# Kernel tuning notes

Measured on AMD Instinct MI355X. Metric: run time of the kernel, lower is better.

Reference implementation:

```python
import jax, jax.numpy as jnp
from jax import lax
import numpy as np

B, R, NOBJ, SIZE = 16, 64, 32, 64  # batch, rels/image, objs/image, map size


def setup_inputs() -> dict:
    key = jax.random.key(0)
    ks = jax.random.split(key, 8)
    # boxes as (x1, y1, x2, y2) in an arbitrary image coordinate frame
    xy1 = jax.random.uniform(ks[0], (B, NOBJ, 2), dtype=jnp.float32) * 80.0
    wh = jax.random.uniform(ks[1], (B, NOBJ, 2), dtype=jnp.float32) * 40.0 + 2.0
    bboxes = jnp.concatenate([xy1, xy1 + wh], axis=-1)  # [B, NOBJ, 4]
    num_obj = jnp.full((B,), NOBJ, dtype=jnp.int32)
    num_relation = jnp.full((B,), R, dtype=jnp.int32)  # constant -> static tot_num_rels
    object_pairs = jax.random.randint(ks[2], (B, R, 2), 0, NOBJ)
    conv1_w = jax.random.normal(ks[3], (64, 2, 5, 5), dtype=jnp.float32) * 0.1
    conv1_b = jnp.zeros((64,), dtype=jnp.float32)
    conv2_w = jax.random.normal(ks[4], (32, 64, 5, 5), dtype=jnp.float32) * 0.05
    conv2_b = jnp.zeros((32,), dtype=jnp.float32)
    fc_w = jax.random.normal(ks[5], (512, 32), dtype=jnp.float32) * 0.1
    fc_b = jnp.zeros((512,), dtype=jnp.float32)
    return dict(bboxes=bboxes, num_obj=num_obj, num_relation=num_relation,
                object_pairs=object_pairs, conv1_w=conv1_w, conv1_b=conv1_b,
                conv2_w=conv2_w, conv2_b=conv2_b, fc_w=fc_w, fc_b=fc_b)


def _sp_maps(bboxes, object_pairs):
    # Vectorized replacement of the per-relation python loop + get_sp:
    # both boxes of a pair are rescaled into the 64x64 frame of their union
    # box and rasterized as binary masks (iCAN-style 2-channel spatial config).
    Bc, Rc, _ = object_pairs.shape
    pairs = object_pairs.reshape(-1, 2)                      # [T, 2]
    b_idx = jnp.repeat(jnp.arange(Bc), Rc)                   # [T]
    b0 = bboxes[b_idx, pairs[:, 0]]                          # [T, 4]
    b1 = bboxes[b_idx, pairs[:, 1]]                          # [T, 4]
    ux1 = jnp.minimum(b0[:, 0], b1[:, 0])
    uy1 = jnp.minimum(b0[:, 1], b1[:, 1])
    ux2 = jnp.maximum(b0[:, 2], b1[:, 2])
    uy2 = jnp.maximum(b0[:, 3], b1[:, 3])
    uw = jnp.maximum(ux2 - ux1, 1e-6)
    uh = jnp.maximum(uy2 - uy1, 1e-6)

    def scale(b):  # union-normalized box in [0, SIZE] grid coords
        return jnp.stack([(b[:, 0] - ux1) / uw * SIZE,
                          (b[:, 1] - uy1) / uh * SIZE,
                          (b[:, 2] - ux1) / uw * SIZE,
                          (b[:, 3] - uy1) / uh * SIZE], axis=-1)

    coords = jnp.arange(SIZE, dtype=jnp.float32) + 0.5
    gx = coords[None, None, :]   # [1, 1, SIZE]
    gy = coords[None, :, None]   # [1, SIZE, 1]

    def rasterize(sb):  # sb: [T, 4] -> [T, SIZE, SIZE]
        x1 = sb[:, 0, None, None]; y1 = sb[:, 1, None, None]
        x2 = sb[:, 2, None, None]; y2 = sb[:, 3, None, None]
        return ((gx >= x1) & (gx <= x2) & (gy >= y1) & (gy <= y2)).astype(jnp.float32)

    return jnp.stack([rasterize(scale(b0)), rasterize(scale(b1))], axis=1)  # [T,2,64,64]


def _conv(x, w, b):
    y = lax.conv_general_dilated(x, w, window_strides=(1, 1), padding='VALID',
                                 dimension_numbers=('NCHW', 'OIHW', 'NCHW'))
    return y + b[None, :, None, None]


def _maxpool2(x):
    return lax.reduce_window(x, -jnp.inf, lax.max, (1, 1, 2, 2), (1, 1, 2, 2), 'VALID')


def reference(bboxes, num_obj, num_relation, object_pairs,
              conv1_w, conv1_b, conv2_w, conv2_b, fc_w, fc_b):
    sp = _sp_maps(bboxes, object_pairs)        # [T, 2, 64, 64]
    x = _maxpool2(_conv(sp, conv1_w, conv1_b)) # [T, 64, 30, 30]
    x = _maxpool2(_conv(x, conv2_w, conv2_b))  # [T, 32, 13, 13]
    x = jnp.mean(x, axis=(2, 3))               # AvgPool((13,13)) -> [T, 32]
    return jax.nn.relu(x @ fc_w.T + fc_b)      # [T, 512]
```

## Files before the change

### kernel.cpp

```cpp
#include <hip/hip_runtime.h>
#include <stdint.h>

typedef unsigned long long u64;
typedef short v8s __attribute__((ext_vector_type(8)));
typedef float v4f __attribute__((ext_vector_type(4)));

__device__ __forceinline__ unsigned short f2bf_rne(float f) {
  union { float f; unsigned u; } c; c.f = f;
  unsigned u = c.u;
  u += 0x7fffu + ((u >> 16) & 1u);
  return (unsigned short)(u >> 16);
}

__device__ __forceinline__ void bacc(uint4 z, uint4 a, float* S) {
  const unsigned* zp = &z.x;
  const unsigned* ap = &a.x;
  #pragma unroll
  for (int k = 0; k < 4; k++) {
    unsigned zu = zp[k], au = ap[k];
    S[2 * k]     += __uint_as_float(zu << 16)         - __uint_as_float(au << 16);
    S[2 * k + 1] += __uint_as_float(zu & 0xffff0000u) - __uint_as_float(au & 0xffff0000u);
  }
}


__global__ __launch_bounds__(512, 8) void conv1_kernel(
    const float* __restrict__ bboxes,
    const int*   __restrict__ pairs,
    const float* __restrict__ w1,
    const float* __restrict__ b1,
    const float* __restrict__ w2,
    unsigned short* __restrict__ XsG,
    unsigned short* __restrict__ Wr)
{
  const int t = threadIdx.x;
  if (blockIdx.x >= 1024) {
    int bb2 = blockIdx.x - 1024;
    #pragma unroll
    for (int r = 0; r < 4; r++) {
      int idx = bb2 * 2048 + r * 512 + t;
      int c = idx / 1600, rem = idx - c * 1600;
      int h = rem / 800, r2 = rem - h * 800;
      int tap = r2 >> 5, chh = r2 & 31;
      Wr[h * 25600 + c * 800 + r2] =
          f2bf_rne(w2[(c * 64 + h * 32 + chh) * 25 + tap]);
    }
    return;
  }
  extern __shared__ char smem[];
  unsigned short* Gs = (unsigned short*)smem;
  float* R = (float*)(smem + 24576);

  const int n = blockIdx.x;
  const int lane = t & 63;

  for (int rid = t; rid < 640; rid += 512) {
    int ch = rid / 320, rr = rid - ch * 320;
    int i = rr >> 6, cout = rr & 63;
    const float* wp = w1 + (cout * 2 + ch) * 25 + i * 5;
    float* Rp = R + (ch * 5 + i) * 384 + cout;
    float s = 0.f;
    #pragma unroll
    for (int j = 0; j < 5; j++) { Rp[j * 64] = s; s += wp[j]; }
    Rp[5 * 64] = s;
  }
  __syncthreads();
  for (int e = t; e < 12288; e += 512) {
    int ch = e / 6144, r = e - ch * 6144;
    int cls = r / 384, r2 = r - cls * 384;
    float v = 0.f;
    if (cls > 0) {
      int ia = 0, ib = 0;
      #pragma unroll
      for (int bb2 = 0; bb2 < 5; bb2++) {
        int base = (bb2 * (bb2 + 1)) / 2 + 1;
        if (cls >= base) { ib = bb2; ia = cls - base; }
      }
      const float* Rp = R + ch * 1920 + r2;
      for (int i = ia; i <= ib; i++) v += Rp[i * 384];
    }
    Gs[e] = f2bf_rne(v);
  }

  const int bb = n >> 6, rr_ = n & 63;
  const int p0 = pairs[(bb * 64 + rr_) * 2 + 0];
  const int p1 = pairs[(bb * 64 + rr_) * 2 + 1];
  const float* A  = bboxes + (bb * 32 + p0) * 4;
  const float* Bq = bboxes + (bb * 32 + p1) * 4;
  const float ax1 = A[0],  ay1 = A[1],  ax2 = A[2],  ay2 = A[3];
  const float cx1 = Bq[0], cy1 = Bq[1], cx2 = Bq[2], cy2 = Bq[3];
  const float ux1 = fminf(ax1, cx1), uy1 = fminf(ay1, cy1);
  const float ux2 = fmaxf(ax2, cx2), uy2 = fmaxf(ay2, cy2);
  const float uw = fmaxf(ux2 - ux1, 1e-6f), uh = fmaxf(uy2 - uy1, 1e-6f);
  const float g = (float)lane + 0.5f;
  u64 ixs[2], iys[2];
  {
    float X1 = (ax1 - ux1) / uw * 64.f, X2 = (ax2 - ux1) / uw * 64.f;
    float Y1 = (ay1 - uy1) / uh * 64.f, Y2 = (ay2 - uy1) / uh * 64.f;
    ixs[0] = __ballot(g >= X1 && g <= X2);
    iys[0] = __ballot(g >= Y1 && g <= Y2);
  }
  {
    float X1 = (cx1 - ux1) / uw * 64.f, X2 = (cx2 - ux1) / uw * 64.f;
    float Y1 = (cy1 - uy1) / uh * 64.f, Y2 = (cy2 - uy1) / uh * 64.f;
    ixs[1] = __ballot(g >= X1 && g <= X2);
    iys[1] = __ballot(g >= Y1 && g <= Y2);
  }
  __syncthreads();

  const int cg = t & 7, cgo = cg * 16, pr = t >> 3;
  const int hW = cg >> 2;
  float b1v[8];
  #pragma unroll
  for (int i = 0; i < 8; i++) b1v[i] = b1[cg * 8 + i];
  char* const Xbase = (char*)XsG + (u64)n * 115200 + hW * 57600;
  for (int pass = 0; pass < 15; pass++) {
    int pix = pr + (pass << 6);
    if (pix < 900) {
      int qy = pix / 30, qx = pix - qy * 30;
      int cb[2][2], ja_[2][2], jb_[2][2];
      #pragma unroll
      for (int ch = 0; ch < 2; ch++) {
        #pragma unroll
        for (int dy = 0; dy < 2; dy++) {
          unsigned m = (unsigned)(iys[ch] >> (2 * qy + dy)) & 31u;
          int ia = __ffs((int)m) - 1; if (ia < 0) ia = 0;
          int ib = 31 - __clz((int)(m | 1u));
          int cls = m ? (((ib * (ib + 1)) >> 1) + ia + 1) : 0;
          cb[ch][dy] = (ch * 16 + cls) * 768 + cgo;
        }
        #pragma unroll
        for (int dx = 0; dx < 2; dx++) {
          unsigned mx = (unsigned)(ixs[ch] >> (2 * qx + dx)) & 31u;
          int ja = __ffs((int)mx) - 1; if (ja < 0) ja = 0;
          int jbp = mx ? (32 - __clz((int)mx)) : 0;
          ja_[ch][dx] = ja * 128; jb_[ch][dx] = jbp * 128;
        }
      }
      float V[8];
      #pragma unroll
      for (int dy = 0; dy < 2; dy++) {
        #pragma unroll
        for (int dx = 0; dx < 2; dx++) {
          float S[8] = {0, 0, 0, 0, 0, 0, 0, 0};
          #pragma unroll
          for (int ch = 0; ch < 2; ch++) {
            uint4 z = *(const uint4*)(smem + cb[ch][dy] + jb_[ch][dx]);
            uint4 a = *(const uint4*)(smem + cb[ch][dy] + ja_[ch][dx]);
            bacc(z, a, S);
          }
          #pragma unroll
          for (int k = 0; k < 8; k++)
            V[k] = (dy == 0 && dx == 0) ? S[k] : fmaxf(V[k], S[k]);
        }
      }
      uint4 pk;
      unsigned* pkp = &pk.x;
      #pragma unroll
      for (int k = 0; k < 4; k++) {
        unsigned lo = (unsigned)f2bf_rne(V[2 * k]     + b1v[2 * k]);
        unsigned hi = (unsigned)f2bf_rne(V[2 * k + 1] + b1v[2 * k + 1]);
        pkp[k] = lo | (hi << 16);
      }
      int slot = ((cg & 3) + pix) & 3;
      *(uint4*)(Xbase + pix * 64 + slot * 16) = pk;
    }
  }
}

__global__ __launch_bounds__(512, 4) void conv2_kernel(
    const unsigned short* __restrict__ XsG,
    const unsigned short* __restrict__ Wr,
    const float* __restrict__ b2,
    const float* __restrict__ fcw,
    const float* __restrict__ fcb,
    float* __restrict__ out)
{
  extern __shared__ char smem[];
  float* partial = (float*)(smem + 57600);
  float* fs      = (float*)(smem + 58432);
  float* Cout    = (float*)smem;

  const int n = blockIdx.x, t = threadIdx.x;
  const int lane = t & 63, wv = t >> 6;
  const int q = lane >> 4, ln = lane & 15;

  v4f acc[6][2];
  int pclamp[6], psB[6];
  int cnt = 0;
  #pragma unroll
  for (int it = 0; it < 6; it++) {
    int nt = wv + it * 8;
    if (nt < 43) {
      int p = nt * 16 + ln; if (p > 675) p = 675;
      pclamp[it] = p;
      int y = p / 26, x = p - y * 26;
      psB[it] = y * 30 + x;
      cnt = it + 1;
    } else { pclamp[it] = 0; psB[it] = 0; }
    acc[it][0] = (v4f)0.f; acc[it][1] = (v4f)0.f;
  }

  const char* Xg = (const char*)XsG + (u64)n * 115200;
  for (int h = 0; h < 2; h++) {
    if (h) __syncthreads();
    {
      const char* src = Xg + h * 57600;
      #pragma unroll
      for (int k = 0; k < 7; k++) {
        int ci = k * 512 + t;
        __builtin_amdgcn_global_load_lds(
            (const __attribute__((address_space(1))) unsigned int*)(src + ci * 16),
            (__attribute__((address_space(3))) unsigned int*)(smem + ci * 16),
            16, 0, 0);
      }
      if (t < 16) {
        int ci = 3584 + t;
        __builtin_amdgcn_global_load_lds(
            (const __attribute__((address_space(1))) unsigned int*)(src + ci * 16),
            (__attribute__((address_space(3))) unsigned int*)(smem + ci * 16),
            16, 0, 0);
      }
    }
    __syncthreads();

    const unsigned short* pA0 = Wr + h * 25600 + ln * 800 + q * 8;
    const unsigned short* pA1 = pA0 + 16 * 800;
    for (int i = 0; i < 5; i++) {
      #pragma unroll
      for (int j = 0; j < 5; j++) {
        const int tap = i * 5 + j;
        v8s a0 = *(const v8s*)(pA0 + tap * 32);
        v8s a1 = *(const v8s*)(pA1 + tap * 32);
        #pragma unroll
        for (int it = 0; it < 6; it++) {
          if (it < cnt) {
            int ps = psB[it] + i * 30 + j;
            int addr = (ps << 6) + (((q + ps) & 3) << 4);
            v8s b = *(const v8s*)(smem + addr);
            acc[it][0] = __builtin_amdgcn_mfma_f32_16x16x32_bf16(a0, b, acc[it][0], 0, 0, 0);
            acc[it][1] = __builtin_amdgcn_mfma_f32_16x16x32_bf16(a1, b, acc[it][1], 0, 0, 0);
          }
        }
      }
    }
  }

  #pragma unroll
  for (int mt = 0; mt < 2; mt++) {
    __syncthreads();
    #pragma unroll
    for (int it = 0; it < 6; it++) {
      if (it < cnt) {
        #pragma unroll
        for (int r = 0; r < 4; r++)
          Cout[(q * 4 + r) * 677 + pclamp[it]] = acc[it][mt][r];
      }
    }
    __syncthreads();
    if (t < 208) {
      int c = t & 15, py = t >> 4;
      const float* r0 = Cout + c * 677 + (2 * py) * 26;
      const float* r1 = r0 + 26;
      float s = 0.f;
      #pragma unroll
      for (int px = 0; px < 13; px++) {
        float m0 = fmaxf(r0[2 * px], r0[2 * px + 1]);
        float m1 = fmaxf(r1[2 * px], r1[2 * px + 1]);
        s += fmaxf(m0, m1);
      }
      partial[t] = s;
    }
    __syncthreads();
    if (t < 16) {
      float s = 0.f;
      #pragma unroll
      for (int k = 0; k < 13; k++) s += partial[k * 16 + t];
      fs[mt * 16 + t] = s * (1.f / 169.f) + b2[mt * 16 + t];
    }
  }
  __syncthreads();

  {
    const float* wrow = fcw + t * 32;
    float d = 0.f;
    #pragma unroll
    for (int k = 0; k < 32; k++) d += wrow[k] * fs[k];
    out[(u64)n * 512 + t] = fmaxf(d + fcb[t], 0.f);
  }
}


__global__ __launch_bounds__(256) void prepack(
    const float* __restrict__ w1, const float* __restrict__ w2,
    unsigned short* __restrict__ Wr, unsigned short* __restrict__ Gt) {
  int idx = blockIdx.x * 256 + threadIdx.x;
  if (idx < 51200) {
    int c = idx / 1600, rem = idx - c * 1600;
    int ch = rem & 63, tap = rem >> 6;
    Wr[idx] = f2bf_rne(w2[(c * 64 + ch) * 25 + tap]);
  } else if (idx < 51200 + 12288) {
    int e = idx - 51200;
    int ch = e / 6144, r = e - ch * 6144;
    int cls = r / 384, r2 = r - cls * 384;
    int j = r2 / 64, cout = r2 - j * 64;
    float v = 0.f;
    if (cls > 0) {
      int ia = 0, ib = 0;
      for (int bb = 0; bb < 5; bb++) {
        int base = (bb * (bb + 1)) / 2 + 1;
        if (cls >= base && cls <= base + bb) { ib = bb; ia = cls - base; }
      }
      for (int i = ia; i <= ib; i++)
        for (int jj = 0; jj < j; jj++)
          v += w1[(cout * 2 + ch) * 25 + i * 5 + jj];
    }
    Gt[e] = f2bf_rne(v);
  }
}

__global__ __launch_bounds__(512, 2) void fused_kernel(
    const float* __restrict__ bboxes, const int* __restrict__ pairs,
    const unsigned short* __restrict__ Gt, const float* __restrict__ b1,
    const unsigned short* __restrict__ Wr, const float* __restrict__ b2,
    const float* __restrict__ fcw, const float* __restrict__ fcb,
    float* __restrict__ out)
{
  extern __shared__ char smem[];
  float* partial = (float*)(smem + 146976);
  float* fs      = (float*)(smem + 147808);
  float* Cout    = (float*)smem;

  const int n = blockIdx.x, t = threadIdx.x;
  const int lane = t & 63, wv = t >> 6;
  const int q = lane >> 4, ln = lane & 15;

  {
    const uint4* src = (const uint4*)Gt;
    uint4* dst = (uint4*)(smem + 122400);
    #pragma unroll
    for (int i = 0; i < 3; i++) dst[t + i * 512] = src[t + i * 512];
  }
  const int bb = n >> 6, rr_ = n & 63;
  const int p0 = pairs[(bb * 64 + rr_) * 2 + 0];
  const int p1 = pairs[(bb * 64 + rr_) * 2 + 1];
  const float* A  = bboxes + (bb * 32 + p0) * 4;
  const float* Bq = bboxes + (bb * 32 + p1) * 4;
  const float ax1 = A[0],  ay1 = A[1],  ax2 = A[2],  ay2 = A[3];
  const float cx1 = Bq[0], cy1 = Bq[1], cx2 = Bq[2], cy2 = Bq[3];
  const float ux1 = fminf(ax1, cx1), uy1 = fminf(ay1, cy1);
  const float ux2 = fmaxf(ax2, cx2), uy2 = fmaxf(ay2, cy2);
  const float uw = fmaxf(ux2 - ux1, 1e-6f), uh = fmaxf(uy2 - uy1, 1e-6f);
  const float g = (float)lane + 0.5f;
  u64 ixs[2], iys[2];
  {
    float X1 = (ax1 - ux1) / uw * 64.f, X2 = (ax2 - ux1) / uw * 64.f;
    float Y1 = (ay1 - uy1) / uh * 64.f, Y2 = (ay2 - uy1) / uh * 64.f;
    ixs[0] = __ballot(g >= X1 && g <= X2);
    iys[0] = __ballot(g >= Y1 && g <= Y2);
  }
  {
    float X1 = (cx1 - ux1) / uw * 64.f, X2 = (cx2 - ux1) / uw * 64.f;
    float Y1 = (cy1 - uy1) / uh * 64.f, Y2 = (cy2 - uy1) / uh * 64.f;
    ixs[1] = __ballot(g >= X1 && g <= X2);
    iys[1] = __ballot(g >= Y1 && g <= Y2);
  }
  __syncthreads();

  {
    const int cg = t & 7, cgo = cg * 16, pr = t >> 3;
    float b1v[8];
    #pragma unroll
    for (int i = 0; i < 8; i++) b1v[i] = b1[cg * 8 + i];
    for (int pass = 0; pass < 15; pass++) {
      int pix = pr + (pass << 6);
      if (pix < 900) {
        int qy = pix / 30, qx = pix - qy * 30;
        int cb[2][2], ja_[2][2], jb_[2][2];
        #pragma unroll
        for (int ch = 0; ch < 2; ch++) {
          #pragma unroll
          for (int dy = 0; dy < 2; dy++) {
            unsigned m = (unsigned)(iys[ch] >> (2 * qy + dy)) & 31u;
            int ia = __ffs((int)m) - 1; if (ia < 0) ia = 0;
            int ib = 31 - __clz((int)(m | 1u));
            int cls = m ? (((ib * (ib + 1)) >> 1) + ia + 1) : 0;
            cb[ch][dy] = 122400 + (ch * 16 + cls) * 768 + cgo;
          }
          #pragma unroll
          for (int dx = 0; dx < 2; dx++) {
            unsigned mx = (unsigned)(ixs[ch] >> (2 * qx + dx)) & 31u;
            int ja = __ffs((int)mx) - 1; if (ja < 0) ja = 0;
            int jbp = mx ? (32 - __clz((int)mx)) : 0;
            ja_[ch][dx] = ja * 128; jb_[ch][dx] = jbp * 128;
          }
        }
        float V[8];
        #pragma unroll
        for (int dy = 0; dy < 2; dy++) {
          #pragma unroll
          for (int dx = 0; dx < 2; dx++) {
            float S[8] = {0, 0, 0, 0, 0, 0, 0, 0};
            #pragma unroll
            for (int ch = 0; ch < 2; ch++) {
              uint4 z = *(const uint4*)(smem + cb[ch][dy] + jb_[ch][dx]);
              uint4 a = *(const uint4*)(smem + cb[ch][dy] + ja_[ch][dx]);
              bacc(z, a, S);
            }
            #pragma unroll
            for (int k = 0; k < 8; k++)
              V[k] = (dy == 0 && dx == 0) ? S[k] : fmaxf(V[k], S[k]);
          }
        }
        unsigned dws[4];
        #pragma unroll
        for (int k = 0; k < 4; k++) {
          unsigned lo = (unsigned)f2bf_rne(V[2 * k]     + b1v[2 * k]);
          unsigned hi = (unsigned)f2bf_rne(V[2 * k + 1] + b1v[2 * k + 1]);
          dws[k] = lo | (hi << 16);
        }
        uint2 s0; s0.x = dws[0]; s0.y = dws[1];
        uint2 s1; s1.x = dws[2]; s1.y = dws[3];
        *(uint2*)(smem + pix * 136 + cgo) = s0;
        *(uint2*)(smem + pix * 136 + cgo + 8) = s1;
      }
    }
  }
  __syncthreads();

  v4f acc[6][2];
  int pclamp[6], baseB[6];
  int cnt = 0;
  #pragma unroll
  for (int it = 0; it < 6; it++) {
    int nt = wv + it * 8;
    if (nt < 43) {
      int p = nt * 16 + ln; if (p > 675) p = 675;
      pclamp[it] = p;
      int y = p / 26, x = p - y * 26;
      baseB[it] = (y * 30 + x) * 136 + q * 16;
      cnt = it + 1;
    } else { pclamp[it] = 0; baseB[it] = 0; }
    acc[it][0] = (v4f)0.f; acc[it][1] = (v4f)0.f;
  }
  const unsigned short* pA0 = Wr + ln * 1600 + q * 8;
  const unsigned short* pA1 = pA0 + 16 * 1600;
  for (int i5 = 0; i5 < 5; i5++) {
    const int ro = i5 * 4080;
    #pragma unroll
    for (int jt = 0; jt < 5; jt++) {
      #pragma unroll
      for (int hh = 0; hh < 2; hh++) {
        const int s = (i5 * 5 + jt) * 2 + hh;
        v8s a0 = *(const v8s*)(pA0 + s * 32);
        v8s a1 = *(const v8s*)(pA1 + s * 32);
        const int off = ro + jt * 136 + hh * 64;
        #pragma unroll
        for (int it = 0; it < 6; it++) {
          if (it < cnt) {
            uint2 lo = *(const uint2*)(smem + (baseB[it] + off));
            uint2 hi = *(const uint2*)(smem + (baseB[it] + off + 8));
            uint4 bv; bv.x = lo.x; bv.y = lo.y; bv.z = hi.x; bv.w = hi.y;
            v8s b = __builtin_bit_cast(v8s, bv);
            acc[it][0] = __builtin_amdgcn_mfma_f32_16x16x32_bf16(a0, b, acc[it][0], 0, 0, 0);
            acc[it][1] = __builtin_amdgcn_mfma_f32_16x16x32_bf16(a1, b, acc[it][1], 0, 0, 0);
          }
        }
      }
    }
  }
  #pragma unroll
  for (int mt = 0; mt < 2; mt++) {
    __syncthreads();
    #pragma unroll
    for (int it = 0; it < 6; it++) {
      if (it < cnt) {
        #pragma unroll
        for (int r = 0; r < 4; r++)
          Cout[(q * 4 + r) * 677 + pclamp[it]] = acc[it][mt][r];
      }
    }
    __syncthreads();
    if (t < 208) {
      int c = t & 15, py = t >> 4;
      const float* r0 = Cout + c * 677 + (2 * py) * 26;
      const float* r1 = r0 + 26;
      float s = 0.f;
      #pragma unroll
      for (int px = 0; px < 13; px++) {
        float m0 = fmaxf(r0[2 * px], r0[2 * px + 1]);
        float m1 = fmaxf(r1[2 * px], r1[2 * px + 1]);
        s += fmaxf(m0, m1);
      }
      partial[t] = s;
    }
    __syncthreads();
    if (t < 16) {
      float s = 0.f;
      #pragma unroll
      for (int k = 0; k < 13; k++) s += partial[k * 16 + t];
      fs[mt * 16 + t] = s * (1.f / 169.f) + b2[mt * 16 + t];
    }
  }
  __syncthreads();
  {
    const float* wrow = fcw + t * 32;
    float d = 0.f;
    #pragma unroll
    for (int k = 0; k < 32; k++) d += wrow[k] * fs[k];
    out[(u64)n * 512 + t] = fmaxf(d + fcb[t], 0.f);
  }
}

extern "C" void kernel_launch(void* const* d_in, const int* in_sizes, int n_in,
                              void* d_out, int out_size, void* d_ws, size_t ws_size,
                              hipStream_t stream) {
  const float* bboxes = (const float*)d_in[0];
  const int*   pairs  = (const int*)  d_in[3];
  const float* w1     = (const float*)d_in[4];
  const float* b1     = (const float*)d_in[5];
  const float* w2     = (const float*)d_in[6];
  const float* b2     = (const float*)d_in[7];
  const float* fcw    = (const float*)d_in[8];
  const float* fcb    = (const float*)d_in[9];
  float* out = (float*)d_out;

  const u64 xs_bytes = (u64)1024 * 115200;
  if (ws_size >= xs_bytes + 102400) {
    unsigned short* XsG = (unsigned short*)d_ws;
    unsigned short* Wr  = (unsigned short*)((char*)d_ws + xs_bytes);
    conv1_kernel<<<1049, 512, 39936, stream>>>(bboxes, pairs, w1, b1, w2, XsG, Wr);
    conv2_kernel<<<1024, 512, 58560, stream>>>(XsG, Wr, b2, fcw, fcb, out);
  } else {
    unsigned short* Wr = (unsigned short*)d_ws;
    unsigned short* Gt = (unsigned short*)((char*)d_ws + 102400);
    prepack<<<248, 256, 0, stream>>>(w1, w2, Wr, Gt);
    fused_kernel<<<1024, 512, 147936, stream>>>(bboxes, pairs, Gt, b1, Wr, b2,
                                                fcw, fcb, out);
  }
}
```

Baseline: 237.0 us.

## Switch conv2 to 32x32x16 MFMA with four 16-channel input chunks

Conv2 now uses the 32x32x16 bf16 MFMA covering all 32 output channels per instruction, instead of pairs of 16x16x32 MFMAs. The conv1 output and the weight prepacking are relaid into four 16-channel input-chunk slabs so each chunk fits in about 29KB of LDS. Halving LDS lets launch bounds rise to 6 blocks per CU, and each B-fragment load now feeds one larger MFMA. The trade-off is four staging rounds with extra syncs instead of two, and a pooling epilogue split into four groups.

Result: slower. 377.1 us (+59.1%).

```diff
diff --git a/kernel.cpp b/kernel.cpp
--- a/kernel.cpp
+++ b/kernel.cpp
@@ -4,6 +4,7 @@
 typedef unsigned long long u64;
 typedef short v8s __attribute__((ext_vector_type(8)));
 typedef float v4f __attribute__((ext_vector_type(4)));
+typedef float v16f __attribute__((ext_vector_type(16)));
 
 __device__ __forceinline__ unsigned short f2bf_rne(float f) {
   union { float f; unsigned u; } c; c.f = f;
@@ -39,11 +40,12 @@
     #pragma unroll
     for (int r = 0; r < 4; r++) {
       int idx = bb2 * 2048 + r * 512 + t;
-      int c = idx / 1600, rem = idx - c * 1600;
-      int h = rem / 800, r2 = rem - h * 800;
-      int tap = r2 >> 5, chh = r2 & 31;
-      Wr[h * 25600 + c * 800 + r2] =
-          f2bf_rne(w2[(c * 64 + h * 32 + chh) * 25 + tap]);
+      int j = idx & 7, v = idx >> 3;
+      int l = v & 63, tapq = v >> 6;
+      int tap = tapq % 25, qq = tapq / 25;
+      int m = l & 31, q2 = l >> 5;
+      int cin = qq * 16 + q2 * 8 + j;
+      Wr[idx] = f2bf_rne(w2[(m * 64 + cin) * 25 + tap]);
     }
     return;
   }
@@ -109,11 +111,11 @@
   __syncthreads();
 
   const int cg = t & 7, cgo = cg * 16, pr = t >> 3;
-  const int hW = cg >> 2;
+  const int qq = cg >> 1, sslot = cg & 1;
   float b1v[8];
   #pragma unroll
   for (int i = 0; i < 8; i++) b1v[i] = b1[cg * 8 + i];
-  char* const Xbase = (char*)XsG + (u64)n * 115200 + hW * 57600;
+  char* const Xbase = (char*)XsG + (u64)n * 115200 + qq * 28800;
   for (int pass = 0; pass < 15; pass++) {
     int pix = pr + (pass << 6);
     if (pix < 900) {
@@ -162,13 +164,13 @@
         unsigned hi = (unsigned)f2bf_rne(V[2 * k + 1] + b1v[2 * k + 1]);
         pkp[k] = lo | (hi << 16);
       }
-      int slot = ((cg & 3) + pix) & 3;
-      *(uint4*)(Xbase + pix * 64 + slot * 16) = pk;
-    }
-  }
-}
-
-__global__ __launch_bounds__(512, 4) void conv2_kernel(
+      int slot = (sslot + (pix >> 2)) & 1;
+      *(uint4*)(Xbase + pix * 32 + slot * 16) = pk;
+    }
+  }
+}
+
+__global__ __launch_bounds__(512, 6) void conv2_kernel(
     const unsigned short* __restrict__ XsG,
     const unsigned short* __restrict__ Wr,
     const float* __restrict__ b2,
@@ -177,45 +179,45 @@
     float* __restrict__ out)
 {
   extern __shared__ char smem[];
-  float* partial = (float*)(smem + 57600);
-  float* fs      = (float*)(smem + 58432);
-  float* Cout    = (float*)smem;
+  float* partial = (float*)(smem + 28800);
+  float* fs      = (float*)(smem + 29632);
+  float* Cout8   = (float*)smem;
 
   const int n = blockIdx.x, t = threadIdx.x;
   const int lane = t & 63, wv = t >> 6;
-  const int q = lane >> 4, ln = lane & 15;
-
-  v4f acc[6][2];
-  int pclamp[6], psB[6];
+  const int n31 = lane & 31, q2 = lane >> 5;
+
+  v16f acc[3];
+  int pclamp[3], psB[3];
   int cnt = 0;
   #pragma unroll
-  for (int it = 0; it < 6; it++) {
+  for (int it = 0; it < 3; it++) {
     int nt = wv + it * 8;
-    if (nt < 43) {
-      int p = nt * 16 + ln; if (p > 675) p = 675;
+    if (nt < 22) {
+      int p = nt * 32 + n31; if (p > 675) p = 675;
       pclamp[it] = p;
       int y = p / 26, x = p - y * 26;
       psB[it] = y * 30 + x;
       cnt = it + 1;
     } else { pclamp[it] = 0; psB[it] = 0; }
-    acc[it][0] = (v4f)0.f; acc[it][1] = (v4f)0.f;
+    acc[it] = (v16f)0.f;
   }
 
   const char* Xg = (const char*)XsG + (u64)n * 115200;
-  for (int h = 0; h < 2; h++) {
-    if (h) __syncthreads();
+  for (int qq = 0; qq < 4; qq++) {
+    if (qq) __syncthreads();
     {
-      const char* src = Xg + h * 57600;
-      #pragma unroll
-      for (int k = 0; k < 7; k++) {
+      const char* src = Xg + qq * 28800;
+      #pragma unroll
+      for (int k = 0; k < 3; k++) {
         int ci = k * 512 + t;
         __builtin_amdgcn_global_load_lds(
             (const __attribute__((address_space(1))) unsigned int*)(src + ci * 16),
             (__attribute__((address_space(3))) unsigned int*)(smem + ci * 16),
             16, 0, 0);
       }
-      if (t < 16) {
-        int ci = 3584 + t;
+      if (t < 264) {
+        int ci = 1536 + t;
         __builtin_amdgcn_global_load_lds(
             (const __attribute__((address_space(1))) unsigned int*)(src + ci * 16),
             (__attribute__((address_space(3))) unsigned int*)(smem + ci * 16),
@@ -224,22 +226,20 @@
     }
     __syncthreads();
 
-    const unsigned short* pA0 = Wr + h * 25600 + ln * 800 + q * 8;
-    const unsigned short* pA1 = pA0 + 16 * 800;
+    const unsigned short* pA = Wr + (u64)(qq * 25 * 64 + lane) * 8;
+    #pragma unroll
     for (int i = 0; i < 5; i++) {
       #pragma unroll
       for (int j = 0; j < 5; j++) {
         const int tap = i * 5 + j;
-        v8s a0 = *(const v8s*)(pA0 + tap * 32);
-        v8s a1 = *(const v8s*)(pA1 + tap * 32);
-        #pragma unroll
-        for (int it = 0; it < 6; it++) {
+        v8s a = *(const v8s*)(pA + tap * 512);
+        #pragma unroll
+        for (int it = 0; it < 3; it++) {
           if (it < cnt) {
-            int ps = psB[it] + i * 30 + j;
-            int addr = (ps << 6) + (((q + ps) & 3) << 4);
+            int p = psB[it] + i * 30 + j;
+            int addr = (p << 5) + (((q2 + (p >> 2)) & 1) << 4);
             v8s b = *(const v8s*)(smem + addr);
-            acc[it][0] = __builtin_amdgcn_mfma_f32_16x16x32_bf16(a0, b, acc[it][0], 0, 0, 0);
-            acc[it][1] = __builtin_amdgcn_mfma_f32_16x16x32_bf16(a1, b, acc[it][1], 0, 0, 0);
+            acc[it] = __builtin_amdgcn_mfma_f32_32x32x16_bf16(a, b, acc[it], 0, 0, 0);
           }
         }
       }
@@ -247,20 +247,20 @@
   }
 
   #pragma unroll
-  for (int mt = 0; mt < 2; mt++) {
-    __syncthreads();
-    #pragma unroll
-    for (int it = 0; it < 6; it++) {
+  for (int gp = 0; gp < 4; gp++) {
+    __syncthreads();
+    #pragma unroll
+    for (int it = 0; it < 3; it++) {
       if (it < cnt) {
         #pragma unroll
-        for (int r = 0; r < 4; r++)
-          Cout[(q * 4 + r) * 677 + pclamp[it]] = acc[it][mt][r];
-      }
-    }
-    __syncthreads();
-    if (t < 208) {
-      int c = t & 15, py = t >> 4;
-      const float* r0 = Cout + c * 677 + (2 * py) * 26;
+        for (int r4 = 0; r4 < 4; r4++)
+          Cout8[(r4 + 4 * q2) * 677 + pclamp[it]] = acc[it][gp * 4 + r4];
+      }
+    }
+    __syncthreads();
+    if (t < 104) {
+      int c = t & 7, py = t >> 3;
+      const float* r0 = Cout8 + c * 677 + (2 * py) * 26;
       const float* r1 = r0 + 26;
       float s = 0.f;
       #pragma unroll
@@ -272,11 +272,11 @@
       partial[t] = s;
     }
     __syncthreads();
-    if (t < 16) {
+    if (t < 8) {
       float s = 0.f;
       #pragma unroll
-      for (int k = 0; k < 13; k++) s += partial[k * 16 + t];
-      fs[mt * 16 + t] = s * (1.f / 169.f) + b2[mt * 16 + t];
+      for (int k = 0; k < 13; k++) s += partial[k * 8 + t];
+      fs[gp * 8 + t] = s * (1.f / 169.f) + b2[gp * 8 + t];
     }
   }
   __syncthreads();
@@ -530,7 +530,7 @@
     unsigned short* XsG = (unsigned short*)d_ws;
     unsigned short* Wr  = (unsigned short*)((char*)d_ws + xs_bytes);
     conv1_kernel<<<1049, 512, 39936, stream>>>(bboxes, pairs, w1, b1, w2, XsG, Wr);
-    conv2_kernel<<<1024, 512, 58560, stream>>>(XsG, Wr, b2, fcw, fcb, out);
+    conv2_kernel<<<1024, 512, 29760, stream>>>(XsG, Wr, b2, fcw, fcb, out);
   } else {
     unsigned short* Wr = (unsigned short*)d_ws;
     unsigned short* Gt = (unsigned short*)((char*)d_ws + 102400);
```

## Pad conv1 output rows to 72 bytes and stage stores through LDS

Applied to the files above, without the earlier changes.

The intermediate activation layout changes from a 64-byte rotated-slot pixel stride to a 72-byte padded stride per pixel. conv1 now writes each pass into a double-buffered LDS tile and then copies it out in contiguous 16-byte chunks, so global stores are coalesced instead of scattered per pixel. conv2 reads the padded layout with two 8-byte LDS loads per fragment to avoid bank conflicts without the XOR swizzle. The cost is more workspace and LDS, an extra barrier per pass in conv1, lower occupancy bounds, and split LDS loads in the MFMA inner loop.

Result: slower. 412.4 us (+74.0%).

```diff
diff --git a/kernel.cpp b/kernel.cpp
--- a/kernel.cpp
+++ b/kernel.cpp
@@ -24,7 +24,7 @@
 }
 
 
-__global__ __launch_bounds__(512, 8) void conv1_kernel(
+__global__ __launch_bounds__(512, 6) void conv1_kernel(
     const float* __restrict__ bboxes,
     const int*   __restrict__ pairs,
     const float* __restrict__ w1,
@@ -50,6 +50,7 @@
   extern __shared__ char smem[];
   unsigned short* Gs = (unsigned short*)smem;
   float* R = (float*)(smem + 24576);
+  char* const bufs = smem + 24576;
 
   const int n = blockIdx.x;
   const int lane = t & 63;
@@ -109,14 +110,17 @@
   __syncthreads();
 
   const int cg = t & 7, cgo = cg * 16, pr = t >> 3;
-  const int hW = cg >> 2;
+  const int h = cg >> 2, sub = cg & 3;
   float b1v[8];
   #pragma unroll
   for (int i = 0; i < 8; i++) b1v[i] = b1[cg * 8 + i];
-  char* const Xbase = (char*)XsG + (u64)n * 115200 + hW * 57600;
+  const u64 imgbase = (u64)n * 129600;
+
   for (int pass = 0; pass < 15; pass++) {
-    int pix = pr + (pass << 6);
-    if (pix < 900) {
+    const int cntpix = (pass == 14) ? 4 : 64;
+    char* buf = bufs + (pass & 1) * 9216;
+    if (pr < cntpix) {
+      int pix = pr + (pass << 6);
       int qy = pix / 30, qx = pix - qy * 30;
       int cb[2][2], ja_[2][2], jb_[2][2];
       #pragma unroll
@@ -162,8 +166,18 @@
         unsigned hi = (unsigned)f2bf_rne(V[2 * k + 1] + b1v[2 * k + 1]);
         pkp[k] = lo | (hi << 16);
       }
-      int slot = ((cg & 3) + pix) & 3;
-      *(uint4*)(Xbase + pix * 64 + slot * 16) = pk;
+      *(uint4*)(buf + h * 4608 + pr * 72 + sub * 16) = pk;
+    }
+    __syncthreads();
+    {
+      const int cph = (cntpix * 9) >> 1;
+      const int tot = cph * 2;
+      for (int idx = t; idx < tot; idx += 512) {
+        int hh = idx >= cph;
+        int off = (idx - hh * cph) * 16;
+        uint4 v = *(const uint4*)(buf + hh * 4608 + off);
+        *(uint4*)((char*)XsG + imgbase + (u64)hh * 64800 + pass * 4608 + off) = v;
+      }
     }
   }
 }
@@ -177,8 +191,8 @@
     float* __restrict__ out)
 {
   extern __shared__ char smem[];
-  float* partial = (float*)(smem + 57600);
-  float* fs      = (float*)(smem + 58432);
+  float* partial = (float*)(smem + 64800);
+  float* fs      = (float*)(smem + 65632);
   float* Cout    = (float*)smem;
 
   const int n = blockIdx.x, t = threadIdx.x;
@@ -186,7 +200,7 @@
   const int q = lane >> 4, ln = lane & 15;
 
   v4f acc[6][2];
-  int pclamp[6], psB[6];
+  int pclamp[6], baseB[6];
   int cnt = 0;
   #pragma unroll
   for (int it = 0; it < 6; it++) {
@@ -195,17 +209,17 @@
       int p = nt * 16 + ln; if (p > 675) p = 675;
       pclamp[it] = p;
       int y = p / 26, x = p - y * 26;
-      psB[it] = y * 30 + x;
+      baseB[it] = (y * 30 + x) * 72 + q * 16;
       cnt = it + 1;
-    } else { pclamp[it] = 0; psB[it] = 0; }
+    } else { pclamp[it] = 0; baseB[it] = 0; }
     acc[it][0] = (v4f)0.f; acc[it][1] = (v4f)0.f;
   }
 
-  const char* Xg = (const char*)XsG + (u64)n * 115200;
+  const char* Xg = (const char*)XsG + (u64)n * 129600;
   for (int h = 0; h < 2; h++) {
     if (h) __syncthreads();
     {
-      const char* src = Xg + h * 57600;
+      const char* src = Xg + h * 64800;
       #pragma unroll
       for (int k = 0; k < 7; k++) {
         int ci = k * 512 + t;
@@ -214,7 +228,7 @@
             (__attribute__((address_space(3))) unsigned int*)(smem + ci * 16),
             16, 0, 0);
       }
-      if (t < 16) {
+      if (t < 466) {
         int ci = 3584 + t;
         __builtin_amdgcn_global_load_lds(
             (const __attribute__((address_space(1))) unsigned int*)(src + ci * 16),
@@ -227,17 +241,20 @@
     const unsigned short* pA0 = Wr + h * 25600 + ln * 800 + q * 8;
     const unsigned short* pA1 = pA0 + 16 * 800;
     for (int i = 0; i < 5; i++) {
+      const int rowoff = i * 2160;
       #pragma unroll
       for (int j = 0; j < 5; j++) {
-        const int tap = i * 5 + j;
-        v8s a0 = *(const v8s*)(pA0 + tap * 32);
-        v8s a1 = *(const v8s*)(pA1 + tap * 32);
+        const int s = i * 5 + j;
+        v8s a0 = *(const v8s*)(pA0 + s * 32);
+        v8s a1 = *(const v8s*)(pA1 + s * 32);
+        const int off = rowoff + j * 72;
         #pragma unroll
         for (int it = 0; it < 6; it++) {
           if (it < cnt) {
-            int ps = psB[it] + i * 30 + j;
-            int addr = (ps << 6) + (((q + ps) & 3) << 4);
-            v8s b = *(const v8s*)(smem + addr);
+            uint2 lo = *(const uint2*)(smem + (baseB[it] + off));
+            uint2 hi = *(const uint2*)(smem + (baseB[it] + off + 8));
+            uint4 bv; bv.x = lo.x; bv.y = lo.y; bv.z = hi.x; bv.w = hi.y;
+            v8s b = __builtin_bit_cast(v8s, bv);
             acc[it][0] = __builtin_amdgcn_mfma_f32_16x16x32_bf16(a0, b, acc[it][0], 0, 0, 0);
             acc[it][1] = __builtin_amdgcn_mfma_f32_16x16x32_bf16(a1, b, acc[it][1], 0, 0, 0);
           }
@@ -525,12 +542,12 @@
   const float* fcb    = (const float*)d_in[9];
   float* out = (float*)d_out;
 
-  const u64 xs_bytes = (u64)1024 * 115200;
+  const u64 xs_bytes = (u64)1024 * 129600;
   if (ws_size >= xs_bytes + 102400) {
     unsigned short* XsG = (unsigned short*)d_ws;
     unsigned short* Wr  = (unsigned short*)((char*)d_ws + xs_bytes);
-    conv1_kernel<<<1049, 512, 39936, stream>>>(bboxes, pairs, w1, b1, w2, XsG, Wr);
-    conv2_kernel<<<1024, 512, 58560, stream>>>(XsG, Wr, b2, fcw, fcb, out);
+    conv1_kernel<<<1049, 512, 43008, stream>>>(bboxes, pairs, w1, b1, w2, XsG, Wr);
+    conv2_kernel<<<1024, 512, 65760, stream>>>(XsG, Wr, b2, fcw, fcb, out);
   } else {
     unsigned short* Wr = (unsigned short*)d_ws;
     unsigned short* Gt = (unsigned short*)((char*)d_ws + 102400);
```
